# Optimization experiments

Measured on AMD Instinct MI355X. Metric: run time of the kernel, lower is better.

Reference implementation:

```python
import jax, jax.numpy as jnp
import numpy as np

N_NODES = 50000
N_FEAT = 256
N_HID = 256
N_CLASS = 40
N_EDGES = 800000


def setup_inputs() -> dict:
    key = jax.random.key(0)
    ks = jax.random.split(key, 12)
    x = jax.random.normal(ks[0], (N_NODES, N_FEAT), dtype=jnp.float32)
    edge_index = jax.random.randint(ks[1], (2, N_EDGES), 0, N_NODES, dtype=jnp.int64)
    def glorot(k, fan_in, fan_out):
        s = jnp.sqrt(6.0 / (fan_in + fan_out)).astype(jnp.float32)
        return jax.random.uniform(k, (fan_in, fan_out), jnp.float32, -s, s)
    return {
        "x": x,
        "edge_index": edge_index,
        "W1": glorot(ks[2], N_FEAT, N_HID), "b1": jnp.zeros((N_HID,), jnp.float32),
        "W2": glorot(ks[3], N_HID, N_HID), "b2": jnp.zeros((N_HID,), jnp.float32),
        "W3": glorot(ks[4], N_HID, N_HID), "b3": jnp.zeros((N_HID,), jnp.float32),
        "W4": glorot(ks[5], N_HID, N_CLASS), "b4": jnp.zeros((N_CLASS,), jnp.float32),
    }


def _gcn_norm(edge_index, num_nodes):
    # add self-loops, compute symmetric normalization (PyG gcn_norm)
    loop = jnp.arange(num_nodes, dtype=edge_index.dtype)
    src = jnp.concatenate([edge_index[0], loop])
    dst = jnp.concatenate([edge_index[1], loop])
    deg = jax.ops.segment_sum(jnp.ones_like(dst, dtype=jnp.float32), dst,
                              num_segments=num_nodes)
    dis = jnp.where(deg > 0, jax.lax.rsqrt(deg), 0.0)
    norm = dis[src] * dis[dst]  # [E + N]
    return src, dst, norm


def _gcn_conv(x, W, b, src, dst, norm, num_nodes):
    h = x @ W  # dense transform first (out_channels <= in_channels)
    msg = norm[:, None] * h[src]  # gather + scale
    out = jax.ops.segment_sum(msg, dst, num_segments=num_nodes)  # scatter-add
    return out + b


def reference(x, edge_index, W1, b1, W2, b2, W3, b3, W4, b4):
    n = x.shape[0]
    src, dst, norm = _gcn_norm(edge_index, n)
    h = jax.nn.relu(_gcn_conv(x, W1, b1, src, dst, norm, n))
    # dropout is identity in eval mode
    h = jax.nn.relu(_gcn_conv(h, W2, b2, src, dst, norm, n))
    h = jax.nn.relu(_gcn_conv(h, W3, b3, src, dst, norm, n))
    out = _gcn_conv(h, W4, b4, src, dst, norm, n)
    return out
```

## Files before the change

### kernel.cpp

```cpp
#include <hip/hip_runtime.h>

#define NN 50000
#define NF 256
#define NH 256
#define NC 40
#define NE 800000

typedef _Float16 f16x8 __attribute__((ext_vector_type(8)));
typedef float f32x4 __attribute__((ext_vector_type(4)));

__device__ __forceinline__ float f16f(unsigned short u) {
  union { unsigned short u; _Float16 h; } a; a.u = u;
  return (float)a.h;
}
__device__ __forceinline__ unsigned short f16u(float f) {
  union { unsigned short u; _Float16 h; } a; a.h = (_Float16)f;
  return a.u;
}

__device__ __forceinline__ void gl16(const void* g, void* l) {
  __builtin_amdgcn_global_load_lds(
      (const __attribute__((address_space(1))) unsigned int*)g,
      (__attribute__((address_space(3))) unsigned int*)l, 16, 0, 0);
}


__global__ void count_kernel(const int* __restrict__ dst, int* __restrict__ cnt) {
  int e = blockIdx.x * blockDim.x + threadIdx.x;
  if (e < NE) atomicAdd(&cnt[dst[e]], 1);
}

__global__ __launch_bounds__(1024) void scan1_kernel(const int* __restrict__ cnt,
                                                     int* __restrict__ row_ptr,
                                                     int* __restrict__ bsum,
                                                     float* __restrict__ dis) {
  __shared__ int s[1024];
  int i = blockIdx.x * 1024 + threadIdx.x;
  int v = (i < NN) ? cnt[i] : 0;
  if (i < NN) dis[i] = rsqrtf((float)(v + 1));
  s[threadIdx.x] = v;
  __syncthreads();
  for (int ofs = 1; ofs < 1024; ofs <<= 1) {
    int t = (threadIdx.x >= ofs) ? s[threadIdx.x - ofs] : 0;
    __syncthreads();
    s[threadIdx.x] += t;
    __syncthreads();
  }
  if (i < NN) row_ptr[i] = s[threadIdx.x] - v;
  if (threadIdx.x == 1023) bsum[blockIdx.x] = s[1023];
}

__global__ __launch_bounds__(1024) void scan23_kernel(int* __restrict__ row_ptr,
                                                      const int* __restrict__ bsum) {
  __shared__ int sb[64];
  const int nb = (NN + 1023) / 1024;
  if (threadIdx.x < 64) {
    int lane = threadIdx.x;
    int v = (lane < nb) ? bsum[lane] : 0;
    for (int ofs = 1; ofs < 64; ofs <<= 1) {
      int t = __shfl_up(v, ofs, 64);
      if (lane >= ofs) v += t;
    }
    sb[lane] = v;
  }
  __syncthreads();
  int i = blockIdx.x * 1024 + threadIdx.x;
  int add = (blockIdx.x > 0) ? sb[blockIdx.x - 1] : 0;
  if (i < NN) row_ptr[i] += add;
  if (i == 0) row_ptr[NN] = NE;
}

__global__ void scatter_kernel(const int* __restrict__ src, const int* __restrict__ dst,
                               const int* __restrict__ row_ptr, int* __restrict__ cur,
                               int2* __restrict__ ew, const float* __restrict__ dis) {
  int e = blockIdx.x * blockDim.x + threadIdx.x;
  if (e < NE) {
    int d = dst[e], s = src[e];
    int pos = row_ptr[d] + atomicAdd(&cur[d], 1);
    int2 v; v.x = s; v.y = __float_as_int(dis[s] * dis[d]);
    ew[pos] = v;
  }
}


__global__ __launch_bounds__(256) void xf16_kernel(const float* __restrict__ x,
                                                   unsigned short* __restrict__ P) {
  int i = blockIdx.x * blockDim.x + threadIdx.x;
  if (i >= NN * NF / 4) return;
  float4 v = ((const float4*)x)[i];
  ushort4 h;
  h.x = f16u(v.x); h.y = f16u(v.y); h.z = f16u(v.z); h.w = f16u(v.w);
  ((ushort4*)P)[i] = h;
}

__global__ void wf16_kernel(const float* __restrict__ W1, const float* __restrict__ W2,
                            const float* __restrict__ W3, const float* __restrict__ W4,
                            unsigned short* __restrict__ Wt1, unsigned short* __restrict__ Wt2,
                            unsigned short* __restrict__ Wt3, unsigned short* __restrict__ Wt4) {
  int idx = blockIdx.x * blockDim.x + threadIdx.x;
  const float* W; unsigned short* Wt; int N;
  if (idx < 65536)       { W = W1; Wt = Wt1; N = 256; }
  else if (idx < 131072) { W = W2; Wt = Wt2; N = 256; idx -= 65536; }
  else if (idx < 196608) { W = W3; Wt = Wt3; N = 256; idx -= 131072; }
  else if (idx < 229376) { W = W4; Wt = Wt4; N = 40;  idx -= 196608; }
  else return;
  int n = idx >> 8, k = idx & 255;
  float v = (n < N) ? W[k * N + n] : 0.0f;
  Wt[idx] = f16u(v);
}


template <int NSTORE>
__global__ __launch_bounds__(256, 2) void gemm_f16(
    const unsigned short* __restrict__ A, const unsigned short* __restrict__ Bt,
    unsigned short* __restrict__ Cout, int M) {
  __shared__ unsigned short lds[2][128 * 64];

  int tid = threadIdx.x;
  int rowBase = blockIdx.x * 128;
  int colBase = blockIdx.y * 128;
  int w = tid >> 6, lane = tid & 63;
  int wr = w >> 1, wc = w & 1;
  int l15 = lane & 15, l4 = lane >> 4;

  f32x4 acc[4][4] = {};

  for (int kt = 0; kt < 4; ++kt) {
#pragma unroll
    for (int c = 0; c < 4; ++c) {
      int gi = c * 256 + tid;
      int row = gi >> 3, gp = gi & 7;
      int gsrc = gp ^ (row & 7);
      int ar = rowBase + row; ar = ar < M ? ar : M - 1;
      int koff = kt * 64 + gsrc * 8;
      gl16(A + (size_t)ar * 256 + koff, &lds[0][gi * 8]);
      int br = colBase + row;
      gl16(Bt + (size_t)br * 256 + koff, &lds[1][gi * 8]);
    }
    __syncthreads();

#pragma unroll
    for (int ks = 0; ks < 2; ++ks) {
      f16x8 a[4], b[4];
      int g = ks * 4 + l4;
#pragma unroll
      for (int mi = 0; mi < 4; ++mi) {
        int row = wr * 64 + mi * 16 + l15;
        int gp = g ^ (row & 7);
        a[mi] = *(const f16x8*)&lds[0][row * 64 + gp * 8];
      }
#pragma unroll
      for (int ni = 0; ni < 4; ++ni) {
        int row = wc * 64 + ni * 16 + l15;
        int gp = g ^ (row & 7);
        b[ni] = *(const f16x8*)&lds[1][row * 64 + gp * 8];
      }
#pragma unroll
      for (int mi = 0; mi < 4; ++mi)
#pragma unroll
        for (int ni = 0; ni < 4; ++ni)
          acc[mi][ni] = __builtin_amdgcn_mfma_f32_16x16x32_f16(a[mi], b[ni], acc[mi][ni], 0, 0, 0);
    }
    __syncthreads();
  }

#pragma unroll
  for (int ni = 0; ni < 4; ++ni) {
    int col = colBase + wc * 64 + ni * 16 + l15;
    if (col < NSTORE) {
#pragma unroll
      for (int mi = 0; mi < 4; ++mi) {
        f32x4 v = acc[mi][ni];
#pragma unroll
        for (int i = 0; i < 4; ++i) {
          int r = rowBase + wr * 64 + mi * 16 + l4 * 4 + i;
          if (r < M) Cout[(size_t)r * NSTORE + col] = f16u(v[i]);
        }
      }
    }
  }
}


__global__ __launch_bounds__(256) void agg256_kernel(
    const unsigned short* __restrict__ T, unsigned short* __restrict__ P,
    const int* __restrict__ rp, const int2* __restrict__ ew,
    const float* __restrict__ dis, const float* __restrict__ b) {
  int node = (blockIdx.x * blockDim.x + threadIdx.x) >> 6;
  int lane = threadIdx.x & 63;
  if (node >= NN) return;
  const ushort4* Tv = (const ushort4*)T;
  float4 bv = ((const float4*)b)[lane];
  float d = dis[node];
  float w0 = d * d;
  ushort4 t = Tv[(size_t)node * 64 + lane];
  float ax = bv.x + w0 * f16f(t.x), ay = bv.y + w0 * f16f(t.y);
  float az = bv.z + w0 * f16f(t.z), aw = bv.w + w0 * f16f(t.w);
  int e = rp[node], end = rp[node + 1];
  for (; e + 4 <= end; e += 4) {
    int2 e0 = ew[e], e1 = ew[e + 1], e2 = ew[e + 2], e3 = ew[e + 3];
    ushort4 t0 = Tv[(size_t)e0.x * 64 + lane];
    ushort4 t1 = Tv[(size_t)e1.x * 64 + lane];
    ushort4 t2 = Tv[(size_t)e2.x * 64 + lane];
    ushort4 t3 = Tv[(size_t)e3.x * 64 + lane];
    float f0 = __int_as_float(e0.y), f1 = __int_as_float(e1.y);
    float f2 = __int_as_float(e2.y), f3 = __int_as_float(e3.y);
    ax += f0 * f16f(t0.x) + f1 * f16f(t1.x) + f2 * f16f(t2.x) + f3 * f16f(t3.x);
    ay += f0 * f16f(t0.y) + f1 * f16f(t1.y) + f2 * f16f(t2.y) + f3 * f16f(t3.y);
    az += f0 * f16f(t0.z) + f1 * f16f(t1.z) + f2 * f16f(t2.z) + f3 * f16f(t3.z);
    aw += f0 * f16f(t0.w) + f1 * f16f(t1.w) + f2 * f16f(t2.w) + f3 * f16f(t3.w);
  }
  for (; e < end; ++e) {
    int2 sw = ew[e];
    float f = __int_as_float(sw.y);
    ushort4 ts = Tv[(size_t)sw.x * 64 + lane];
    ax += f * f16f(ts.x); ay += f * f16f(ts.y);
    az += f * f16f(ts.z); aw += f * f16f(ts.w);
  }
  ax = fmaxf(ax, 0.f); ay = fmaxf(ay, 0.f);
  az = fmaxf(az, 0.f); aw = fmaxf(aw, 0.f);
  ushort4 h;
  h.x = f16u(ax); h.y = f16u(ay); h.z = f16u(az); h.w = f16u(aw);
  ((ushort4*)P)[(size_t)node * 64 + lane] = h;
}

__global__ __launch_bounds__(256) void agg40_kernel(
    const unsigned short* __restrict__ T, float* __restrict__ O,
    const int* __restrict__ rp, const int2* __restrict__ ew,
    const float* __restrict__ dis, const float* __restrict__ b) {
  int node = (blockIdx.x * blockDim.x + threadIdx.x) >> 6;
  int lane = threadIdx.x & 63;
  if (node >= NN) return;
  float d = dis[node];
  int e = rp[node], end = rp[node + 1];
  if (lane < NC) {
    float acc = b[lane] + d * d * f16f(T[(size_t)node * NC + lane]);
    for (; e + 4 <= end; e += 4) {
      int2 e0 = ew[e], e1 = ew[e + 1], e2 = ew[e + 2], e3 = ew[e + 3];
      float t0 = f16f(T[(size_t)e0.x * NC + lane]);
      float t1 = f16f(T[(size_t)e1.x * NC + lane]);
      float t2 = f16f(T[(size_t)e2.x * NC + lane]);
      float t3 = f16f(T[(size_t)e3.x * NC + lane]);
      acc += __int_as_float(e0.y) * t0 + __int_as_float(e1.y) * t1 +
             __int_as_float(e2.y) * t2 + __int_as_float(e3.y) * t3;
    }
    for (; e < end; ++e) {
      int2 sw = ew[e];
      acc += __int_as_float(sw.y) * f16f(T[(size_t)sw.x * NC + lane]);
    }
    O[(size_t)node * NC + lane] = acc;
  }
}


extern "C" void kernel_launch(void* const* d_in, const int* in_sizes, int n_in,
                              void* d_out, int out_size, void* d_ws, size_t ws_size,
                              hipStream_t stream) {
  const float* x  = (const float*)d_in[0];
  const int* edge = (const int*)d_in[1];
  const float* W1 = (const float*)d_in[2];
  const float* b1 = (const float*)d_in[3];
  const float* W2 = (const float*)d_in[4];
  const float* b2 = (const float*)d_in[5];
  const float* W3 = (const float*)d_in[6];
  const float* b3 = (const float*)d_in[7];
  const float* W4 = (const float*)d_in[8];
  const float* b4 = (const float*)d_in[9];
  float* out = (float*)d_out;

  char* p = (char*)d_ws;
  unsigned short* T16 = (unsigned short*)p; p += (size_t)NN * NH * 2;
  unsigned short* P16 = (unsigned short*)p; p += (size_t)NN * NH * 2;
  int* cnt = (int*)p;                p += (size_t)NN * 4;
  int* cur = (int*)p;                p += (size_t)NN * 4;
  float* dis = (float*)p;            p += (size_t)NN * 4;
  int* row_ptr = (int*)p;            p += (size_t)(NN + 16) * 4;
  int* bsum = (int*)p;               p += 256 * 4;
  int2* ew = (int2*)p;               p += (size_t)NE * 8;
  unsigned short* Wt1 = (unsigned short*)p; p += 256 * 256 * 2;
  unsigned short* Wt2 = (unsigned short*)p; p += 256 * 256 * 2;
  unsigned short* Wt3 = (unsigned short*)p; p += 256 * 256 * 2;
  unsigned short* Wt4 = (unsigned short*)p; p += 128 * 256 * 2;

  const int* e_src = edge;
  const int* e_dst = edge + NE;

  hipMemsetAsync(cnt, 0, (size_t)NN * 8, stream);

  const int nb1024 = (NN + 1023) / 1024;
  count_kernel<<<(NE + 255) / 256, 256, 0, stream>>>(e_dst, cnt);
  scan1_kernel<<<nb1024, 1024, 0, stream>>>(cnt, row_ptr, bsum, dis);
  scan23_kernel<<<nb1024, 1024, 0, stream>>>(row_ptr, bsum);
  scatter_kernel<<<(NE + 255) / 256, 256, 0, stream>>>(e_src, e_dst, row_ptr, cur, ew, dis);

  xf16_kernel<<<(NN * NF / 4 + 255) / 256, 256, 0, stream>>>(x, P16);
  wf16_kernel<<<(229376 + 255) / 256, 256, 0, stream>>>(W1, W2, W3, W4, Wt1, Wt2, Wt3, Wt4);

  dim3 gFull((NN + 127) / 128, 2);
  dim3 gLast((NN + 127) / 128, 1);
  int aggBlocks = (NN * 64 + 255) / 256;

  gemm_f16<256><<<gFull, 256, 0, stream>>>(P16, Wt1, T16, NN);
  agg256_kernel<<<aggBlocks, 256, 0, stream>>>(T16, P16, row_ptr, ew, dis, b1);
  gemm_f16<256><<<gFull, 256, 0, stream>>>(P16, Wt2, T16, NN);
  agg256_kernel<<<aggBlocks, 256, 0, stream>>>(T16, P16, row_ptr, ew, dis, b2);
  gemm_f16<256><<<gFull, 256, 0, stream>>>(P16, Wt3, T16, NN);
  agg256_kernel<<<aggBlocks, 256, 0, stream>>>(T16, P16, row_ptr, ew, dis, b3);
  gemm_f16<NC><<<gLast, 256, 0, stream>>>(P16, Wt4, T16, NN);
  agg40_kernel<<<aggBlocks, 256, 0, stream>>>(T16, out, row_ptr, ew, dis, b4);
}
```

Before: 381.9 us.

## Fuse fp32-to-fp16 input conversion into first GEMM and double-buffer LDS tiles

Removes the separate kernel that converts x to fp16. The first GEMM now loads fp32 rows directly, converts them in registers and writes fp16 into LDS, which avoids a full write and re-read of the fp16 copy of x. The GEMM also gains a two-stage LDS double buffer, so the next K-tile's loads are issued before the MFMAs on the current tile. This doubles LDS use per block to 64 KB and makes the first layer's A loads synchronous register loads rather than async LDS DMA.

```diff
diff --git a/kernel.cpp b/kernel.cpp
--- a/kernel.cpp
+++ b/kernel.cpp
@@ -83,16 +83,6 @@
 }
 
 
-__global__ __launch_bounds__(256) void xf16_kernel(const float* __restrict__ x,
-                                                   unsigned short* __restrict__ P) {
-  int i = blockIdx.x * blockDim.x + threadIdx.x;
-  if (i >= NN * NF / 4) return;
-  float4 v = ((const float4*)x)[i];
-  ushort4 h;
-  h.x = f16u(v.x); h.y = f16u(v.y); h.z = f16u(v.z); h.w = f16u(v.w);
-  ((ushort4*)P)[i] = h;
-}
-
 __global__ void wf16_kernel(const float* __restrict__ W1, const float* __restrict__ W2,
                             const float* __restrict__ W3, const float* __restrict__ W4,
                             unsigned short* __restrict__ Wt1, unsigned short* __restrict__ Wt2,
@@ -110,11 +100,11 @@
 }
 
 
-template <int NSTORE>
+template <int NSTORE, bool AF32>
 __global__ __launch_bounds__(256, 2) void gemm_f16(
-    const unsigned short* __restrict__ A, const unsigned short* __restrict__ Bt,
+    const void* __restrict__ Ain, const unsigned short* __restrict__ Bt,
     unsigned short* __restrict__ Cout, int M) {
-  __shared__ unsigned short lds[2][128 * 64];
+  __shared__ unsigned short lds[2][2][128 * 64];
 
   int tid = threadIdx.x;
   int rowBase = blockIdx.x * 128;
@@ -125,19 +115,35 @@
 
   f32x4 acc[4][4] = {};
 
-  for (int kt = 0; kt < 4; ++kt) {
+  auto stage = [&](int kt, int buf) {
 #pragma unroll
     for (int c = 0; c < 4; ++c) {
       int gi = c * 256 + tid;
       int row = gi >> 3, gp = gi & 7;
       int gsrc = gp ^ (row & 7);
+      int koff = kt * 64 + gsrc * 8;
       int ar = rowBase + row; ar = ar < M ? ar : M - 1;
-      int koff = kt * 64 + gsrc * 8;
-      gl16(A + (size_t)ar * 256 + koff, &lds[0][gi * 8]);
+      if (AF32) {
+        const float* Af = (const float*)Ain + (size_t)ar * 256 + koff;
+        float4 v0 = *(const float4*)Af;
+        float4 v1 = *(const float4*)(Af + 4);
+        f16x8 h = {(_Float16)v0.x, (_Float16)v0.y, (_Float16)v0.z, (_Float16)v0.w,
+                   (_Float16)v1.x, (_Float16)v1.y, (_Float16)v1.z, (_Float16)v1.w};
+        *(f16x8*)&lds[buf][0][gi * 8] = h;
+      } else {
+        gl16((const unsigned short*)Ain + (size_t)ar * 256 + koff, &lds[buf][0][gi * 8]);
+      }
       int br = colBase + row;
-      gl16(Bt + (size_t)br * 256 + koff, &lds[1][gi * 8]);
-    }
-    __syncthreads();
+      gl16(Bt + (size_t)br * 256 + koff, &lds[buf][1][gi * 8]);
+    }
+  };
+
+  stage(0, 0);
+  __syncthreads();
+
+  for (int kt = 0; kt < 4; ++kt) {
+    int buf = kt & 1;
+    if (kt < 3) stage(kt + 1, buf ^ 1);
 
 #pragma unroll
     for (int ks = 0; ks < 2; ++ks) {
@@ -147,13 +153,13 @@
       for (int mi = 0; mi < 4; ++mi) {
         int row = wr * 64 + mi * 16 + l15;
         int gp = g ^ (row & 7);
-        a[mi] = *(const f16x8*)&lds[0][row * 64 + gp * 8];
+        a[mi] = *(const f16x8*)&lds[buf][0][row * 64 + gp * 8];
       }
 #pragma unroll
       for (int ni = 0; ni < 4; ++ni) {
         int row = wc * 64 + ni * 16 + l15;
         int gp = g ^ (row & 7);
-        b[ni] = *(const f16x8*)&lds[1][row * 64 + gp * 8];
+        b[ni] = *(const f16x8*)&lds[buf][1][row * 64 + gp * 8];
       }
 #pragma unroll
       for (int mi = 0; mi < 4; ++mi)
@@ -293,19 +299,18 @@
   scan23_kernel<<<nb1024, 1024, 0, stream>>>(row_ptr, bsum);
   scatter_kernel<<<(NE + 255) / 256, 256, 0, stream>>>(e_src, e_dst, row_ptr, cur, ew, dis);
 
-  xf16_kernel<<<(NN * NF / 4 + 255) / 256, 256, 0, stream>>>(x, P16);
   wf16_kernel<<<(229376 + 255) / 256, 256, 0, stream>>>(W1, W2, W3, W4, Wt1, Wt2, Wt3, Wt4);
 
   dim3 gFull((NN + 127) / 128, 2);
   dim3 gLast((NN + 127) / 128, 1);
   int aggBlocks = (NN * 64 + 255) / 256;
 
-  gemm_f16<256><<<gFull, 256, 0, stream>>>(P16, Wt1, T16, NN);
+  gemm_f16<256, true><<<gFull, 256, 0, stream>>>(x, Wt1, T16, NN);
   agg256_kernel<<<aggBlocks, 256, 0, stream>>>(T16, P16, row_ptr, ew, dis, b1);
-  gemm_f16<256><<<gFull, 256, 0, stream>>>(P16, Wt2, T16, NN);
+  gemm_f16<256, false><<<gFull, 256, 0, stream>>>(P16, Wt2, T16, NN);
   agg256_kernel<<<aggBlocks, 256, 0, stream>>>(T16, P16, row_ptr, ew, dis, b2);
-  gemm_f16<256><<<gFull, 256, 0, stream>>>(P16, Wt3, T16, NN);
+  gemm_f16<256, false><<<gFull, 256, 0, stream>>>(P16, Wt3, T16, NN);
   agg256_kernel<<<aggBlocks, 256, 0, stream>>>(T16, P16, row_ptr, ew, dis, b3);
-  gemm_f16<NC><<<gLast, 256, 0, stream>>>(P16, Wt4, T16, NN);
+  gemm_f16<NC, false><<<gLast, 256, 0, stream>>>(P16, Wt4, T16, NN);
   agg40_kernel<<<aggBlocks, 256, 0, stream>>>(T16, out, row_ptr, ew, dis, b4);
 }
```

New measurement: 378.7 us. Within noise of the previous version (-0.8%).
